# Kernel optimization log

Hardware: AMD Instinct MI355X
Metric: run time of the kernel (lower is better)

The kernel has to match this reference:

```python
import jax, jax.numpy as jnp
import numpy as np

B, A, C = 16, 16384, 81
TOP_K = 50
CONF_THRESH = 0.5
IOU_THRESH = 0.5
VAR0, VAR1 = 0.1, 0.2          # cfg['variance']
IMG_HW = 1.0                   # cfg['min_dim']/img_size = 320/320
MIN_SIZE = 0.0
NEG = -jnp.inf


def setup_inputs() -> dict:
    key = jax.random.key(0)
    k1, k2, k3 = jax.random.split(key, 3)
    conf_preds = jax.random.uniform(k1, (B, A, C), dtype=jnp.float32)
    loc_delta = jax.random.normal(k2, (B, A, 4), dtype=jnp.float32)
    anchors = jax.random.uniform(k3, (A, 4), dtype=jnp.float32)  # cxcywh priors in [0,1)
    return {"conf_preds": conf_preds, "loc_delta": loc_delta, "anchors": anchors}


def _decode_clip(loc, anchors):
    # SSD decode: cxcy = prior_cxcy + loc_xy*v0*prior_wh ; wh = prior_wh*exp(loc_wh*v1)
    cxcy = anchors[..., :2] + loc[..., :2] * VAR0 * anchors[..., 2:]
    wh = anchors[..., 2:] * jnp.exp(loc[..., 2:] * VAR1)
    x1y1 = cxcy - wh * 0.5
    x2y2 = x1y1 + wh
    boxes = jnp.concatenate([x1y1, x2y2], axis=-1)  # [..., 4] xyxy
    return jnp.clip(boxes, 0.0, IMG_HW)            # clip_boxes_to_image((1,1))


def _nms_single(boxes, s):
    # boxes: [A,4] xyxy, s: [A] scores with invalid entries already at -inf.
    # Greedy NMS, fixed TOP_K iterations (torchvision semantics: suppress iou > thresh).
    areas = (boxes[:, 2] - boxes[:, 0]) * (boxes[:, 3] - boxes[:, 1])

    def step(s, _):
        i = jnp.argmax(s)
        take = s[i] > NEG
        b = boxes[i]
        xx1 = jnp.maximum(b[0], boxes[:, 0])
        yy1 = jnp.maximum(b[1], boxes[:, 1])
        xx2 = jnp.minimum(b[2], boxes[:, 2])
        yy2 = jnp.minimum(b[3], boxes[:, 3])
        inter = jnp.maximum(xx2 - xx1, 0.0) * jnp.maximum(yy2 - yy1, 0.0)
        iou = inter / (areas[i] + areas - inter)
        s = jnp.where(take & (iou > IOU_THRESH), NEG, s)
        s = s.at[i].set(NEG)  # guarantee progress
        return s, (i, take)

    _, (idx, take) = jax.lax.scan(step, s, None, length=TOP_K)
    return idx, take  # [TOP_K] int, [TOP_K] bool


def reference(conf_preds, loc_delta, anchors):
    boxes = _decode_clip(loc_delta, anchors)                # [B,A,4]
    conf = jnp.transpose(conf_preds, (0, 2, 1))             # [B,C,A]
    # remove_small_boxes(min_size=0) as a mask (all-true here, kept for fidelity)
    w = boxes[..., 2] - boxes[..., 0]
    h = boxes[..., 3] - boxes[..., 1]
    valid = (w >= MIN_SIZE) & (h >= MIN_SIZE)               # [B,A]
    masked = jnp.where((conf > CONF_THRESH) & valid[:, None, :], conf, NEG)  # [B,C,A]

    sg = jax.lax.stop_gradient
    nms_c = jax.vmap(_nms_single, in_axes=(None, 0))        # over classes
    nms_bc = jax.vmap(nms_c, in_axes=(0, 0))                # over batch
    idx, take = nms_bc(sg(boxes), sg(masked))               # [B,C,K]

    scores_sel = jnp.take_along_axis(conf, idx, axis=2)     # [B,C,K]
    b_idx = jnp.arange(boxes.shape[0])[:, None, None]
    boxes_sel = boxes[b_idx, idx]                           # [B,C,K,4]
    preds = jnp.concatenate([
        jnp.where(take, scores_sel, 0.0)[..., None],
        jnp.where(take[..., None], boxes_sel, 0.0),
    ], axis=-1)                                             # [B,C,K,5]
    return preds
```

## Files before the change

### kernel.cpp

```cpp
#include <hip/hip_runtime.h>
#include <math.h>

#define NB 16
#define NA 16384
#define NC 81
#define TOPK 50
#define TRC 4096
#define NEGF (-__builtin_inff())
#define SUPC 0.5000000298023223876953125

typedef unsigned long long ull;

#define WS_CONFT_OFF  ((size_t)4194304)
#define WS_FULL  (WS_CONFT_OFF + (size_t)NB * NC * NA * 4)
#define WS_HALF  (WS_CONFT_OFF + (size_t)8  * NC * NA * 4)

__global__ __launch_bounds__(256) void decode_k(const float* __restrict__ loc,
                                                const float* __restrict__ anc,
                                                float* __restrict__ boxes) {
#pragma clang fp contract(off)
    int i = blockIdx.x * 256 + threadIdx.x;
    if (i >= NB * NA) return;
    int a = i & (NA - 1);
    float4 an = ((const float4*)anc)[a];
    float4 ld = ((const float4*)loc)[i];
    float cx = an.x + (ld.x * 0.1f) * an.z;
    float cy = an.y + (ld.y * 0.1f) * an.w;
    float w = an.z * (float)exp((double)(ld.z * 0.2f));
    float h = an.w * (float)exp((double)(ld.w * 0.2f));
    float x1 = cx - w * 0.5f;
    float y1 = cy - h * 0.5f;
    float x2 = x1 + w;
    float y2 = y1 + h;
    x1 = fminf(fmaxf(x1, 0.f), 1.f);
    y1 = fminf(fmaxf(y1, 0.f), 1.f);
    x2 = fminf(fmaxf(x2, 0.f), 1.f);
    y2 = fminf(fmaxf(y2, 0.f), 1.f);
    ((float4*)boxes)[i] = make_float4(x1, y1, x2, y2);
}

#define TSLAB 64
__global__ __launch_bounds__(256) void transpose_k(const float* __restrict__ conf,
                                                   float* __restrict__ confT, int b0) {
    __shared__ float lin[TSLAB * NC];
    const int bl = blockIdx.y;
    const int b = b0 + bl;
    const int a0 = blockIdx.x * TSLAB;
    const float4* src = (const float4*)(conf + ((size_t)b * NA + a0) * NC);
    const int t = threadIdx.x;
    for (int i = t; i < (TSLAB * NC) / 4; i += 256) {
        float4 v = src[i];
        lin[4 * i + 0] = v.x; lin[4 * i + 1] = v.y;
        lin[4 * i + 2] = v.z; lin[4 * i + 3] = v.w;
    }
    __syncthreads();
    const int x = t & 63, cg = t >> 6;
    float* dst = confT + (size_t)bl * NC * NA + a0 + x;
    for (int c = cg; c < NC; c += 4)
        dst[(size_t)c * NA] = lin[x * NC + c];
}

__global__ __launch_bounds__(256, 8) void nmsB3_k(const float* __restrict__ confT,
                                                  const float* __restrict__ boxes,
                                                  float* __restrict__ out, int b0) {
#pragma clang fp contract(off)
    const int blk = blockIdx.x;
    const int bl = blk / NC, c = blk - bl * NC;
    const int b = b0 + bl;
    const int t = threadIdx.x;
    const int lane = t & 63, wv = t >> 6;

    __shared__ unsigned short s_ix[TRC];
    __shared__ unsigned s_off[513];
    __shared__ unsigned s_aux[512];
    __shared__ float s_acc[TOPK][5];
    __shared__ float4 s_cbox[256];
    __shared__ unsigned long long s_kill[4];
    __shared__ int s_ctrl[16];

    const float* row = confT + ((size_t)bl * NC + c) * NA;
    const float4* row4 = (const float4*)row;
    const float4* bb = (const float4*)boxes + (size_t)b * NA;
    float* orow = out + ((size_t)b * NC + c) * (TOPK * 5);

    for (int i = t; i < 512; i += 256) s_aux[i] = 0u;
    if (t == 0) { s_ctrl[0] = 0; s_ctrl[8] = 0; s_ctrl[12] = 0; }
    __syncthreads();
#pragma unroll 4
    for (int r = 0; r < 16; ++r) {
        float4 v4 = row4[t + 256 * r];
        if (v4.x > 0.5f) atomicAdd(&s_aux[511u - ((__float_as_uint(v4.x) >> 14) & 0x1FFu)], 1u);
        if (v4.y > 0.5f) atomicAdd(&s_aux[511u - ((__float_as_uint(v4.y) >> 14) & 0x1FFu)], 1u);
        if (v4.z > 0.5f) atomicAdd(&s_aux[511u - ((__float_as_uint(v4.z) >> 14) & 0x1FFu)], 1u);
        if (v4.w > 0.5f) atomicAdd(&s_aux[511u - ((__float_as_uint(v4.w) >> 14) & 0x1FFu)], 1u);
    }
    __syncthreads();
    for (int i = t; i < 512; i += 256) atomicMax(&s_ctrl[8], (int)s_aux[i]);
    if (t == 0) s_off[0] = 0u;
    for (int i = t; i < 512; i += 256) s_off[i + 1] = s_aux[i];
    __syncthreads();
    for (int d = 1; d < 512; d <<= 1) {
        int i0 = 1 + t, i1 = 257 + t;
        unsigned v0 = (i0 - d >= 1) ? s_off[i0 - d] : 0u;
        unsigned v1 = (i1 - d >= 1) ? s_off[i1 - d] : 0u;
        __syncthreads();
        s_off[i0] += v0;
        s_off[i1] += v1;
        __syncthreads();
    }

    if (s_ctrl[8] <= TRC) {
        while (true) {
            if (t == 0) {
                int lo = s_ctrl[12];
                int hi = lo;
                while (hi < 512 && s_off[hi + 1] - s_off[lo] <= (unsigned)TRC) hi++;
                s_ctrl[13] = hi;
            }
            __syncthreads();
            const int trLo = s_ctrl[12], trHi = s_ctrl[13];
            const unsigned tbase = s_off[trLo], tend = s_off[trHi];
            if (tbase == tend) break;
            for (int i = trLo + t; i < trHi; i += 256) s_aux[i] = s_off[i] - tbase;
            __syncthreads();
#pragma unroll 4
            for (int r = 0; r < 16; ++r) {
                float4 v4 = row4[t + 256 * r];
                int a0i = 4 * (t + 256 * r);
                if (v4.x > 0.5f) { int bk = (int)(511u - ((__float_as_uint(v4.x) >> 14) & 0x1FFu)); if (bk >= trLo && bk < trHi) s_ix[atomicAdd(&s_aux[bk], 1u)] = (unsigned short)(a0i + 0); }
                if (v4.y > 0.5f) { int bk = (int)(511u - ((__float_as_uint(v4.y) >> 14) & 0x1FFu)); if (bk >= trLo && bk < trHi) s_ix[atomicAdd(&s_aux[bk], 1u)] = (unsigned short)(a0i + 1); }
                if (v4.z > 0.5f) { int bk = (int)(511u - ((__float_as_uint(v4.z) >> 14) & 0x1FFu)); if (bk >= trLo && bk < trHi) s_ix[atomicAdd(&s_aux[bk], 1u)] = (unsigned short)(a0i + 2); }
                if (v4.w > 0.5f) { int bk = (int)(511u - ((__float_as_uint(v4.w) >> 14) & 0x1FFu)); if (bk >= trLo && bk < trHi) s_ix[atomicAdd(&s_aux[bk], 1u)] = (unsigned short)(a0i + 3); }
            }
            if (t == 0) s_ctrl[7] = trLo;
            __syncthreads();

            while (true) {
                if (t == 0) {
                    int bp = s_ctrl[7];
                    int mode;
                    if (bp >= trHi || s_off[bp] >= tend) {
                        mode = 2;
                    } else {
                        unsigned pos = s_off[bp] - tbase;
                        int bpl = bp;
                        unsigned q = pos;
                        for (int w = 0; w < 4; ++w) {
                            s_ctrl[2 + w] = (int)q;
                            while (bpl < trHi && (s_off[bpl + 1] - tbase - q) <= 64u) bpl++;
                            q = (bpl < trHi) ? s_off[bpl] - tbase : tend - tbase;
                        }
                        s_ctrl[6] = (int)q;
                        s_ctrl[7] = bpl;
                        mode = 0;
                        if (q == pos) {
                            mode = 1;
                            s_ctrl[9] = (int)pos;
                            s_ctrl[10] = (int)(s_off[bp + 1] - tbase);
                            s_ctrl[7] = bp + 1;
                        }
                    }
                    s_ctrl[11] = mode;
                }
                __syncthreads();
                const int mode = s_ctrl[11];
                if (mode == 2) break;
                const int nacc0 = s_ctrl[0];

                if (mode == 0) {
                    const unsigned q0 = (unsigned)s_ctrl[2 + wv];
                    const unsigned q1 = (unsigned)s_ctrl[3 + wv];
                    const int mw = (int)(q1 - q0);
                    const bool valid = lane < mw;
                    int ii = (int)q0 + lane; if (ii > TRC - 1) ii = TRC - 1;
                    int a = valid ? (int)s_ix[ii] : 0;
                    float4 bxv = bb[a];
                    if (!valid) bxv = make_float4(0.f, 0.f, 0.f, 0.f);
                    s_cbox[wv * 64 + lane] = bxv;
                    float mar = (bxv.z - bxv.x) * (bxv.w - bxv.y);
                    bool kill = !valid;
                    for (int j = 0; j < nacc0; ++j) {
                        float xx1 = fmaxf(s_acc[j][0], bxv.x), yy1 = fmaxf(s_acc[j][1], bxv.y);
                        float xx2 = fminf(s_acc[j][2], bxv.z), yy2 = fminf(s_acc[j][3], bxv.w);
                        float iw = fmaxf(xx2 - xx1, 0.f), ih = fmaxf(yy2 - yy1, 0.f);
                        float inter = iw * ih;
                        float den = (s_acc[j][4] + mar) - inter;
                        if ((double)inter > (double)den * SUPC) kill = true;
                    }
                    unsigned long long km = __ballot(kill);
                    if (lane == 0) s_kill[wv] = km;
                    __syncthreads();

                    if (wv == 0) {
                        int na = nacc0;
                        for (int cc = 0; cc < 4 && na < TOPK; ++cc) {
                            const unsigned e0 = (unsigned)s_ctrl[2 + cc];
                            const unsigned e1 = (unsigned)s_ctrl[3 + cc];
                            const int mc = (int)(e1 - e0);
                            if (mc <= 0) continue;
                            unsigned long long alive = ~s_kill[cc];
                            if (mc < 64) alive &= (1ull << mc) - 1ull;
                            int jj = (int)e0 + lane; if (jj > TRC - 1) jj = TRC - 1;
                            int aj = (lane < mc) ? (int)s_ix[jj] : 0;
                            float myscore = row[aj];
                            float4 mybx = s_cbox[cc * 64 + lane];
                            float mar2 = (mybx.z - mybx.x) * (mybx.w - mybx.y);
                            for (int j = nacc0; j < na && alive; ++j) {
                                float xx1 = fmaxf(s_acc[j][0], mybx.x), yy1 = fmaxf(s_acc[j][1], mybx.y);
                                float xx2 = fminf(s_acc[j][2], mybx.z), yy2 = fminf(s_acc[j][3], mybx.w);
                                float iw = fmaxf(xx2 - xx1, 0.f), ih = fmaxf(yy2 - yy1, 0.f);
                                float inter = iw * ih;
                                float den = (s_acc[j][4] + mar2) - inter;
                                bool sup = ((double)inter > (double)den * SUPC);
                                alive &= ~__ballot(sup);
                            }
                            unsigned long long mykey =
                                ((unsigned long long)__float_as_uint(myscore) << 32) |
                                (unsigned)(16383 - aj);
                            while (alive && na < TOPK) {
                                unsigned long long kk = ((alive >> lane) & 1ull) ? mykey : 0ull;
                                int src = lane;
                                for (int off = 32; off; off >>= 1) {
                                    unsigned long long ok = __shfl_xor(kk, off);
                                    int osrc = __shfl_xor(src, off);
                                    if (ok > kk) { kk = ok; src = osrc; }
                                }
                                float4 wb = s_cbox[cc * 64 + src];
                                float wscore = __shfl(myscore, src);
                                float war = (wb.z - wb.x) * (wb.w - wb.y);
                                if (lane == 0) {
                                    orow[na * 5 + 0] = wscore;
                                    orow[na * 5 + 1] = wb.x; orow[na * 5 + 2] = wb.y;
                                    orow[na * 5 + 3] = wb.z; orow[na * 5 + 4] = wb.w;
                                    s_acc[na][0] = wb.x; s_acc[na][1] = wb.y;
                                    s_acc[na][2] = wb.z; s_acc[na][3] = wb.w;
                                    s_acc[na][4] = war;
                                }
                                na++;
                                alive &= ~(1ull << src);
                                if (alive) {
                                    float xx1 = fmaxf(wb.x, mybx.x), yy1 = fmaxf(wb.y, mybx.y);
                                    float xx2 = fminf(wb.z, mybx.z), yy2 = fminf(wb.w, mybx.w);
                                    float iw = fmaxf(xx2 - xx1, 0.f), ih = fmaxf(yy2 - yy1, 0.f);
                                    float inter = iw * ih;
                                    float den = (war + mar2) - inter;
                                    bool sup = ((double)inter > (double)den * SUPC);
                                    alive &= ~__ballot(sup);
                                }
                            }
                        }
                        if (lane == 0) s_ctrl[0] = na;
                    }
                    __syncthreads();
                } else {
                    const int e0 = s_ctrl[9], e1 = s_ctrl[10];
                    if (wv == 0) {
                        int na = s_ctrl[0];
                        while (na < TOPK) {
                            unsigned long long bk = 0ull; int bpos = 0;
                            for (int i = e0 + lane; i < e1; i += 64) {
                                int av = (int)s_ix[i];
                                if (av != 0xFFFF) {
                                    float v = row[av];
                                    unsigned long long k =
                                        ((unsigned long long)__float_as_uint(v) << 32) |
                                        (unsigned)(16383 - av);
                                    if (k > bk) { bk = k; bpos = i; }
                                }
                            }
                            for (int off = 32; off; off >>= 1) {
                                unsigned long long ok = __shfl_xor(bk, off);
                                int op = __shfl_xor(bpos, off);
                                if (ok > bk) { bk = ok; bpos = op; }
                            }
                            if (bk == 0ull) break;
                            int a = (int)s_ix[bpos];
                            float wscore = __uint_as_float((unsigned)(bk >> 32));
                            if (lane == 0) s_ix[bpos] = 0xFFFFu;
                            float4 wb = bb[a];
                            float war = (wb.z - wb.x) * (wb.w - wb.y);
                            bool sup = false;
                            if (lane < na) {
                                float xx1 = fmaxf(s_acc[lane][0], wb.x), yy1 = fmaxf(s_acc[lane][1], wb.y);
                                float xx2 = fminf(s_acc[lane][2], wb.z), yy2 = fminf(s_acc[lane][3], wb.w);
                                float iw = fmaxf(xx2 - xx1, 0.f), ih = fmaxf(yy2 - yy1, 0.f);
                                float inter = iw * ih;
                                float den = (s_acc[lane][4] + war) - inter;
                                sup = ((double)inter > (double)den * SUPC);
                            }
                            if (__ballot(sup) == 0ull) {
                                if (lane == 0) {
                                    orow[na * 5 + 0] = wscore;
                                    orow[na * 5 + 1] = wb.x; orow[na * 5 + 2] = wb.y;
                                    orow[na * 5 + 3] = wb.z; orow[na * 5 + 4] = wb.w;
                                    s_acc[na][0] = wb.x; s_acc[na][1] = wb.y;
                                    s_acc[na][2] = wb.z; s_acc[na][3] = wb.w;
                                    s_acc[na][4] = war;
                                }
                                na++;
                            }
                        }
                        if (lane == 0) s_ctrl[0] = na;
                    }
                    __syncthreads();
                }
                if (s_ctrl[0] >= TOPK) break;
            }
            if (s_ctrl[0] >= TOPK || trHi >= 512) break;
            if (t == 0) s_ctrl[12] = trHi;
            __syncthreads();
        }
    } else {
        float hi = 1.0f, delta = 0.02f;
        while (true) {
            if (s_ctrl[0] >= TOPK || hi <= 0.5f) break;
            float lo = fmaxf(hi - delta, 0.5f);
            if (t == 0) s_ctrl[1] = 0;
            __syncthreads();
            for (int r = 0; r < 16; ++r) {
                float4 v4 = row4[t + 256 * r];
                int a0i = 4 * (t + 256 * r);
                if (v4.x > lo && v4.x <= hi) { int p = atomicAdd(&s_ctrl[1], 1); if (p < TRC) s_ix[p] = (unsigned short)(a0i + 0); }
                if (v4.y > lo && v4.y <= hi) { int p = atomicAdd(&s_ctrl[1], 1); if (p < TRC) s_ix[p] = (unsigned short)(a0i + 1); }
                if (v4.z > lo && v4.z <= hi) { int p = atomicAdd(&s_ctrl[1], 1); if (p < TRC) s_ix[p] = (unsigned short)(a0i + 2); }
                if (v4.w > lo && v4.w <= hi) { int p = atomicAdd(&s_ctrl[1], 1); if (p < TRC) s_ix[p] = (unsigned short)(a0i + 3); }
            }
            __syncthreads();
            int m = s_ctrl[1];
            if (m > TRC) { delta *= 0.5f; continue; }
            if (wv == 0) {
                int na = s_ctrl[0];
                while (na < TOPK) {
                    unsigned long long bk = 0ull; int bpos = 0;
                    for (int i = lane; i < m; i += 64) {
                        int av = (int)s_ix[i];
                        if (av != 0xFFFF) {
                            float v = row[av];
                            unsigned long long k =
                                ((unsigned long long)__float_as_uint(v) << 32) |
                                (unsigned)(16383 - av);
                            if (k > bk) { bk = k; bpos = i; }
                        }
                    }
                    for (int off = 32; off; off >>= 1) {
                        unsigned long long ok = __shfl_xor(bk, off);
                        int op = __shfl_xor(bpos, off);
                        if (ok > bk) { bk = ok; bpos = op; }
                    }
                    if (bk == 0ull) break;
                    int a = (int)s_ix[bpos];
                    float wscore = __uint_as_float((unsigned)(bk >> 32));
                    if (lane == 0) s_ix[bpos] = 0xFFFFu;
                    float4 wb = bb[a];
                    float war = (wb.z - wb.x) * (wb.w - wb.y);
                    bool sup = false;
                    if (lane < na) {
                        float xx1 = fmaxf(s_acc[lane][0], wb.x), yy1 = fmaxf(s_acc[lane][1], wb.y);
                        float xx2 = fminf(s_acc[lane][2], wb.z), yy2 = fminf(s_acc[lane][3], wb.w);
                        float iw = fmaxf(xx2 - xx1, 0.f), ih = fmaxf(yy2 - yy1, 0.f);
                        float inter = iw * ih;
                        float den = (s_acc[lane][4] + war) - inter;
                        sup = ((double)inter > (double)den * SUPC);
                    }
                    if (__ballot(sup) == 0ull) {
                        if (lane == 0) {
                            orow[na * 5 + 0] = wscore;
                            orow[na * 5 + 1] = wb.x; orow[na * 5 + 2] = wb.y;
                            orow[na * 5 + 3] = wb.z; orow[na * 5 + 4] = wb.w;
                            s_acc[na][0] = wb.x; s_acc[na][1] = wb.y;
                            s_acc[na][2] = wb.z; s_acc[na][3] = wb.w;
                            s_acc[na][4] = war;
                        }
                        na++;
                    }
                }
                if (lane == 0) s_ctrl[0] = na;
            }
            __syncthreads();
            hi = lo;
        }
    }

    __syncthreads();
    const int naF = s_ctrl[0];
    for (int z = naF * 5 + t; z < TOPK * 5; z += 256) orow[z] = 0.f;
}

#define OTHREADS 1024
#define OCAP 10240
#define OJMAX 10

__global__ __launch_bounds__(OTHREADS) void nms_old_k(const float* __restrict__ conf,
                                                      const float* __restrict__ boxes,
                                                      float* __restrict__ out) {
#pragma clang fp contract(off)
    const int blk = blockIdx.x;
    const int b = blk / NC, c = blk - b * NC;
    const int t = threadIdx.x;
    const int lane = t & 63, wid = t >> 6;
    __shared__ float s_val[OCAP];
    __shared__ unsigned short s_idx[OCAP];
    __shared__ float s_ps[2][16];
    __shared__ int s_pa[2][16];
    __shared__ int s_n;
    if (t == 0) s_n = 0;
    __syncthreads();
    const float* cp = conf + ((size_t)b * NA) * NC + c;
    float v[NA / OTHREADS];
#pragma unroll
    for (int r = 0; r < NA / OTHREADS; ++r)
        v[r] = cp[(size_t)(r * OTHREADS + t) * NC];
#pragma unroll
    for (int r = 0; r < NA / OTHREADS; ++r) {
        int a = r * OTHREADS + t;
        bool alive = v[r] > 0.5f;
        unsigned long long m = __ballot(alive);
        int cnt = __popcll(m);
        int base = 0;
        if (lane == 0 && cnt) base = atomicAdd(&s_n, cnt);
        base = __shfl(base, 0);
        if (alive) {
            int p = base + __popcll(m & ((1ull << lane) - 1));
            if (p < OCAP) { s_val[p] = v[r]; s_idx[p] = (unsigned short)a; }
        }
    }
    __syncthreads();
    int n = s_n; if (n > OCAP) n = OCAP;
    const int jn = (n + OTHREADS - 1) / OTHREADS;
    const float4* bb = (const float4*)boxes + (size_t)b * NA;
    float sc[OJMAX]; float4 bx[OJMAX]; int ia[OJMAX];
#pragma unroll
    for (int j = 0; j < OJMAX; ++j) {
        sc[j] = NEGF; ia[j] = 0x7fffffff; bx[j] = make_float4(0.f, 0.f, 0.f, 0.f);
        int p = j * OTHREADS + t;
        if (p < n) { sc[j] = s_val[p]; ia[j] = (int)s_idx[p]; bx[j] = bb[ia[j]]; }
    }
    float* orow = out + (size_t)blk * (TOPK * 5);
    int k = 0;
    for (; k < TOPK; ++k) {
        float ms = NEGF; int ma = 0x7fffffff;
#pragma unroll
        for (int j = 0; j < OJMAX; ++j) {
            if (j < jn) {
                bool better = (sc[j] > ms) || (sc[j] == ms && ia[j] < ma);
                ms = better ? sc[j] : ms;
                ma = better ? ia[j] : ma;
            }
        }
#pragma unroll
        for (int off = 32; off; off >>= 1) {
            float os = __shfl_xor(ms, off);
            int oa = __shfl_xor(ma, off);
            if (os > ms || (os == ms && oa < ma)) { ms = os; ma = oa; }
        }
        int pb = k & 1;
        if (lane == 0) { s_ps[pb][wid] = ms; s_pa[pb][wid] = ma; }
        __syncthreads();
        float wsv = NEGF; int wa = 0x7fffffff;
#pragma unroll
        for (int w = 0; w < 16; ++w) {
            float os = s_ps[pb][w]; int oa = s_pa[pb][w];
            if (os > wsv || (os == wsv && oa < wa)) { wsv = os; wa = oa; }
        }
        if (!(wsv > NEGF)) break;
        float4 wb = bb[wa];
        float warea = (wb.z - wb.x) * (wb.w - wb.y);
        if (t == 0) {
            orow[k * 5 + 0] = wsv;
            orow[k * 5 + 1] = wb.x; orow[k * 5 + 2] = wb.y;
            orow[k * 5 + 3] = wb.z; orow[k * 5 + 4] = wb.w;
        }
#pragma unroll
        for (int j = 0; j < OJMAX; ++j) {
            if (j < jn) {
                float xx1 = fmaxf(wb.x, bx[j].x);
                float yy1 = fmaxf(wb.y, bx[j].y);
                float xx2 = fminf(wb.z, bx[j].z);
                float yy2 = fminf(wb.w, bx[j].w);
                float iw = fmaxf(xx2 - xx1, 0.f);
                float ih = fmaxf(yy2 - yy1, 0.f);
                float inter = iw * ih;
                float aj = (bx[j].z - bx[j].x) * (bx[j].w - bx[j].y);
                float denom = (warea + aj) - inter;
                bool supp = ((double)inter > (double)denom * SUPC) || (ia[j] == wa);
                if (supp) sc[j] = NEGF;
            }
        }
    }
    for (int z = k * 5 + t; z < TOPK * 5; z += OTHREADS) orow[z] = 0.f;
}

extern "C" void kernel_launch(void* const* d_in, const int* in_sizes, int n_in,
                              void* d_out, int out_size, void* d_ws, size_t ws_size,
                              hipStream_t stream) {
    const float* conf = (const float*)d_in[0];
    const float* loc  = (const float*)d_in[1];
    const float* anc  = (const float*)d_in[2];
    float* boxes = (float*)d_ws;

    decode_k<<<(NB * NA + 255) / 256, 256, 0, stream>>>(loc, anc, boxes);

    if (ws_size >= WS_FULL) {
        float* confT = (float*)((char*)d_ws + WS_CONFT_OFF);
        dim3 tg(NA / TSLAB, NB);
        transpose_k<<<tg, 256, 0, stream>>>(conf, confT, 0);
        nmsB3_k<<<NB * NC, 256, 0, stream>>>(confT, boxes, (float*)d_out, 0);
    } else if (ws_size >= WS_HALF) {
        float* confT = (float*)((char*)d_ws + WS_CONFT_OFF);
        for (int h = 0; h < 2; ++h) {
            dim3 tg(NA / TSLAB, 8);
            transpose_k<<<tg, 256, 0, stream>>>(conf, confT, h * 8);
            nmsB3_k<<<8 * NC, 256, 0, stream>>>(confT, boxes, (float*)d_out, h * 8);
        }
    } else {
        nms_old_k<<<NB * NC, OTHREADS, 0, stream>>>(conf, boxes, (float*)d_out);
    }
}
```

Baseline: 232.8 us.

## Store transposed confidences as 16-bit bucket codes and read scores from original layout

The transpose kernel now writes a 16-bit histogram-bucket code per (class, anchor) instead of the full float score, using 256-anchor slabs. This halves the transposed buffer size and its write and read traffic, and the NMS kernel's histogram and scatter passes read 8 codes per 16-byte load. Exact scores for the few candidates are fetched with strided reads from the original conf tensor. The fallback threshold-scan path now does fully strided scalar reads of conf, and the half-workspace branch is removed.

Result: no change. 231.1 us (-0.7%).

```diff
diff --git a/kernel.cpp b/kernel.cpp
--- a/kernel.cpp
+++ b/kernel.cpp
@@ -12,8 +12,7 @@
 typedef unsigned long long ull;
 
 #define WS_CONFT_OFF  ((size_t)4194304)
-#define WS_FULL  (WS_CONFT_OFF + (size_t)NB * NC * NA * 4)
-#define WS_HALF  (WS_CONFT_OFF + (size_t)8  * NC * NA * 4)
+#define WS_FULL  (WS_CONFT_OFF + (size_t)NB * NC * NA * 2)
 
 __global__ __launch_bounds__(256) void decode_k(const float* __restrict__ loc,
                                                 const float* __restrict__ anc,
@@ -39,34 +38,48 @@
     ((float4*)boxes)[i] = make_float4(x1, y1, x2, y2);
 }
 
-#define TSLAB 64
-__global__ __launch_bounds__(256) void transpose_k(const float* __restrict__ conf,
-                                                   float* __restrict__ confT, int b0) {
-    __shared__ float lin[TSLAB * NC];
-    const int bl = blockIdx.y;
-    const int b = b0 + bl;
-    const int a0 = blockIdx.x * TSLAB;
-    const float4* src = (const float4*)(conf + ((size_t)b * NA + a0) * NC);
+__device__ __forceinline__ unsigned short enc_code(float v) {
+    unsigned short e = 0xFFFFu;
+    if (v > 0.5f) e = (unsigned short)(511u - ((__float_as_uint(v) >> 14) & 0x1FFu));
+    return e;
+}
+
+#define TSLAB 256
+__global__ __launch_bounds__(256) void transq_k(const float* __restrict__ conf,
+                                                unsigned short* __restrict__ confT) {
+    __shared__ unsigned short code[TSLAB * NC];
+    const int b = blockIdx.y;
+    const int slab = blockIdx.x;
+    const float4* src = (const float4*)(conf + ((size_t)b * NA + (size_t)slab * TSLAB) * NC);
     const int t = threadIdx.x;
     for (int i = t; i < (TSLAB * NC) / 4; i += 256) {
         float4 v = src[i];
-        lin[4 * i + 0] = v.x; lin[4 * i + 1] = v.y;
-        lin[4 * i + 2] = v.z; lin[4 * i + 3] = v.w;
-    }
-    __syncthreads();
-    const int x = t & 63, cg = t >> 6;
-    float* dst = confT + (size_t)bl * NC * NA + a0 + x;
-    for (int c = cg; c < NC; c += 4)
-        dst[(size_t)c * NA] = lin[x * NC + c];
+        unsigned f = 4u * (unsigned)i;
+        unsigned a = f / (unsigned)NC;
+        unsigned c = f - a * (unsigned)NC;
+        code[c * TSLAB + a] = enc_code(v.x);
+        if (++c == NC) { c = 0; ++a; }
+        code[c * TSLAB + a] = enc_code(v.y);
+        if (++c == NC) { c = 0; ++a; }
+        code[c * TSLAB + a] = enc_code(v.z);
+        if (++c == NC) { c = 0; ++a; }
+        code[c * TSLAB + a] = enc_code(v.w);
+    }
+    __syncthreads();
+    const int lane = t & 63, wv = t >> 6;
+    for (int c = wv; c < NC; c += 4) {
+        ull v = *(const ull*)&code[c * TSLAB + lane * 4];
+        *(ull*)(confT + ((size_t)b * NC + c) * NA + (size_t)slab * TSLAB + lane * 4) = v;
+    }
 }
 
-__global__ __launch_bounds__(256, 8) void nmsB3_k(const float* __restrict__ confT,
+__global__ __launch_bounds__(256, 8) void nmsB4_k(const unsigned short* __restrict__ confT,
+                                                  const float* __restrict__ conf,
                                                   const float* __restrict__ boxes,
-                                                  float* __restrict__ out, int b0) {
+                                                  float* __restrict__ out) {
 #pragma clang fp contract(off)
     const int blk = blockIdx.x;
-    const int bl = blk / NC, c = blk - bl * NC;
-    const int b = b0 + bl;
+    const int b = blk / NC, c = blk - b * NC;
     const int t = threadIdx.x;
     const int lane = t & 63, wv = t >> 6;
 
@@ -78,21 +91,26 @@
     __shared__ unsigned long long s_kill[4];
     __shared__ int s_ctrl[16];
 
-    const float* row = confT + ((size_t)bl * NC + c) * NA;
-    const float4* row4 = (const float4*)row;
+    const uint4* row8 = (const uint4*)(confT + ((size_t)b * NC + c) * NA);
+    const float* cp = conf + ((size_t)b * NA) * NC + c;
     const float4* bb = (const float4*)boxes + (size_t)b * NA;
     float* orow = out + ((size_t)b * NC + c) * (TOPK * 5);
 
     for (int i = t; i < 512; i += 256) s_aux[i] = 0u;
     if (t == 0) { s_ctrl[0] = 0; s_ctrl[8] = 0; s_ctrl[12] = 0; }
     __syncthreads();
-#pragma unroll 4
-    for (int r = 0; r < 16; ++r) {
-        float4 v4 = row4[t + 256 * r];
-        if (v4.x > 0.5f) atomicAdd(&s_aux[511u - ((__float_as_uint(v4.x) >> 14) & 0x1FFu)], 1u);
-        if (v4.y > 0.5f) atomicAdd(&s_aux[511u - ((__float_as_uint(v4.y) >> 14) & 0x1FFu)], 1u);
-        if (v4.z > 0.5f) atomicAdd(&s_aux[511u - ((__float_as_uint(v4.z) >> 14) & 0x1FFu)], 1u);
-        if (v4.w > 0.5f) atomicAdd(&s_aux[511u - ((__float_as_uint(v4.w) >> 14) & 0x1FFu)], 1u);
+#pragma unroll
+    for (int r = 0; r < 8; ++r) {
+        uint4 q = row8[t + 256 * r];
+        unsigned w;
+        w = q.x; if ((w & 0xFFFFu) != 0xFFFFu) atomicAdd(&s_aux[w & 0xFFFFu], 1u);
+                 if ((w >> 16)     != 0xFFFFu) atomicAdd(&s_aux[w >> 16], 1u);
+        w = q.y; if ((w & 0xFFFFu) != 0xFFFFu) atomicAdd(&s_aux[w & 0xFFFFu], 1u);
+                 if ((w >> 16)     != 0xFFFFu) atomicAdd(&s_aux[w >> 16], 1u);
+        w = q.z; if ((w & 0xFFFFu) != 0xFFFFu) atomicAdd(&s_aux[w & 0xFFFFu], 1u);
+                 if ((w >> 16)     != 0xFFFFu) atomicAdd(&s_aux[w >> 16], 1u);
+        w = q.w; if ((w & 0xFFFFu) != 0xFFFFu) atomicAdd(&s_aux[w & 0xFFFFu], 1u);
+                 if ((w >> 16)     != 0xFFFFu) atomicAdd(&s_aux[w >> 16], 1u);
     }
     __syncthreads();
     for (int i = t; i < 512; i += 256) atomicMax(&s_ctrl[8], (int)s_aux[i]);
@@ -123,14 +141,23 @@
             if (tbase == tend) break;
             for (int i = trLo + t; i < trHi; i += 256) s_aux[i] = s_off[i] - tbase;
             __syncthreads();
-#pragma unroll 4
-            for (int r = 0; r < 16; ++r) {
-                float4 v4 = row4[t + 256 * r];
-                int a0i = 4 * (t + 256 * r);
-                if (v4.x > 0.5f) { int bk = (int)(511u - ((__float_as_uint(v4.x) >> 14) & 0x1FFu)); if (bk >= trLo && bk < trHi) s_ix[atomicAdd(&s_aux[bk], 1u)] = (unsigned short)(a0i + 0); }
-                if (v4.y > 0.5f) { int bk = (int)(511u - ((__float_as_uint(v4.y) >> 14) & 0x1FFu)); if (bk >= trLo && bk < trHi) s_ix[atomicAdd(&s_aux[bk], 1u)] = (unsigned short)(a0i + 1); }
-                if (v4.z > 0.5f) { int bk = (int)(511u - ((__float_as_uint(v4.z) >> 14) & 0x1FFu)); if (bk >= trLo && bk < trHi) s_ix[atomicAdd(&s_aux[bk], 1u)] = (unsigned short)(a0i + 2); }
-                if (v4.w > 0.5f) { int bk = (int)(511u - ((__float_as_uint(v4.w) >> 14) & 0x1FFu)); if (bk >= trLo && bk < trHi) s_ix[atomicAdd(&s_aux[bk], 1u)] = (unsigned short)(a0i + 3); }
+#pragma unroll
+            for (int r = 0; r < 8; ++r) {
+                uint4 q = row8[t + 256 * r];
+                int a0i = 8 * (t + 256 * r);
+                unsigned w; int bk;
+                w = q.x;
+                bk = (int)(w & 0xFFFFu); if (bk >= trLo && bk < trHi) s_ix[atomicAdd(&s_aux[bk], 1u)] = (unsigned short)(a0i + 0);
+                bk = (int)(w >> 16);     if (bk >= trLo && bk < trHi) s_ix[atomicAdd(&s_aux[bk], 1u)] = (unsigned short)(a0i + 1);
+                w = q.y;
+                bk = (int)(w & 0xFFFFu); if (bk >= trLo && bk < trHi) s_ix[atomicAdd(&s_aux[bk], 1u)] = (unsigned short)(a0i + 2);
+                bk = (int)(w >> 16);     if (bk >= trLo && bk < trHi) s_ix[atomicAdd(&s_aux[bk], 1u)] = (unsigned short)(a0i + 3);
+                w = q.z;
+                bk = (int)(w & 0xFFFFu); if (bk >= trLo && bk < trHi) s_ix[atomicAdd(&s_aux[bk], 1u)] = (unsigned short)(a0i + 4);
+                bk = (int)(w >> 16);     if (bk >= trLo && bk < trHi) s_ix[atomicAdd(&s_aux[bk], 1u)] = (unsigned short)(a0i + 5);
+                w = q.w;
+                bk = (int)(w & 0xFFFFu); if (bk >= trLo && bk < trHi) s_ix[atomicAdd(&s_aux[bk], 1u)] = (unsigned short)(a0i + 6);
+                bk = (int)(w >> 16);     if (bk >= trLo && bk < trHi) s_ix[atomicAdd(&s_aux[bk], 1u)] = (unsigned short)(a0i + 7);
             }
             if (t == 0) s_ctrl[7] = trLo;
             __syncthreads();
@@ -202,7 +229,7 @@
                             if (mc < 64) alive &= (1ull << mc) - 1ull;
                             int jj = (int)e0 + lane; if (jj > TRC - 1) jj = TRC - 1;
                             int aj = (lane < mc) ? (int)s_ix[jj] : 0;
-                            float myscore = row[aj];
+                            float myscore = cp[(size_t)aj * NC];
                             float4 mybx = s_cbox[cc * 64 + lane];
                             float mar2 = (mybx.z - mybx.x) * (mybx.w - mybx.y);
                             for (int j = nacc0; j < na && alive; ++j) {
@@ -261,7 +288,7 @@
                             for (int i = e0 + lane; i < e1; i += 64) {
                                 int av = (int)s_ix[i];
                                 if (av != 0xFFFF) {
-                                    float v = row[av];
+                                    float v = cp[(size_t)av * NC];
                                     unsigned long long k =
                                         ((unsigned long long)__float_as_uint(v) << 32) |
                                         (unsigned)(16383 - av);
@@ -317,13 +344,12 @@
             float lo = fmaxf(hi - delta, 0.5f);
             if (t == 0) s_ctrl[1] = 0;
             __syncthreads();
-            for (int r = 0; r < 16; ++r) {
-                float4 v4 = row4[t + 256 * r];
-                int a0i = 4 * (t + 256 * r);
-                if (v4.x > lo && v4.x <= hi) { int p = atomicAdd(&s_ctrl[1], 1); if (p < TRC) s_ix[p] = (unsigned short)(a0i + 0); }
-                if (v4.y > lo && v4.y <= hi) { int p = atomicAdd(&s_ctrl[1], 1); if (p < TRC) s_ix[p] = (unsigned short)(a0i + 1); }
-                if (v4.z > lo && v4.z <= hi) { int p = atomicAdd(&s_ctrl[1], 1); if (p < TRC) s_ix[p] = (unsigned short)(a0i + 2); }
-                if (v4.w > lo && v4.w <= hi) { int p = atomicAdd(&s_ctrl[1], 1); if (p < TRC) s_ix[p] = (unsigned short)(a0i + 3); }
+            for (int a = t; a < NA; a += 256) {
+                float v = cp[(size_t)a * NC];
+                if (v > lo && v <= hi) {
+                    int p = atomicAdd(&s_ctrl[1], 1);
+                    if (p < TRC) s_ix[p] = (unsigned short)a;
+                }
             }
             __syncthreads();
             int m = s_ctrl[1];
@@ -335,7 +361,7 @@
                     for (int i = lane; i < m; i += 64) {
                         int av = (int)s_ix[i];
                         if (av != 0xFFFF) {
-                            float v = row[av];
+                            float v = cp[(size_t)av * NC];
                             unsigned long long k =
                                 ((unsigned long long)__float_as_uint(v) << 32) |
                                 (unsigned)(16383 - av);
@@ -501,17 +527,10 @@
     decode_k<<<(NB * NA + 255) / 256, 256, 0, stream>>>(loc, anc, boxes);
 
     if (ws_size >= WS_FULL) {
-        float* confT = (float*)((char*)d_ws + WS_CONFT_OFF);
+        unsigned short* confT = (unsigned short*)((char*)d_ws + WS_CONFT_OFF);
         dim3 tg(NA / TSLAB, NB);
-        transpose_k<<<tg, 256, 0, stream>>>(conf, confT, 0);
-        nmsB3_k<<<NB * NC, 256, 0, stream>>>(confT, boxes, (float*)d_out, 0);
-    } else if (ws_size >= WS_HALF) {
-        float* confT = (float*)((char*)d_ws + WS_CONFT_OFF);
-        for (int h = 0; h < 2; ++h) {
-            dim3 tg(NA / TSLAB, 8);
-            transpose_k<<<tg, 256, 0, stream>>>(conf, confT, h * 8);
-            nmsB3_k<<<8 * NC, 256, 0, stream>>>(confT, boxes, (float*)d_out, h * 8);
-        }
+        transq_k<<<tg, 256, 0, stream>>>(conf, confT);
+        nmsB4_k<<<NB * NC, 256, 0, stream>>>(confT, conf, boxes, (float*)d_out);
     } else {
         nms_old_k<<<NB * NC, OTHREADS, 0, stream>>>(conf, boxes, (float*)d_out);
     }
```
